# Performance work log

Measured on AMD Instinct MI355X. Metric: run time of the kernel, lower is better.

The kernel has to match this reference:

```python
import jax, jax.numpy as jnp
import numpy as np

ATOM_DIM = 64
BOND_DIM = 64
B, N_ATOMS, N_BONDS = 32, 256, 512


def setup_inputs() -> dict:
    key = jax.random.key(0)
    k1, k2, k3, k4 = jax.random.split(key, 4)
    atom_state = jax.random.normal(k1, (B, N_ATOMS, ATOM_DIM), dtype=jnp.float32)
    bond_state = jax.random.normal(k2, (B, N_BONDS, BOND_DIM), dtype=jnp.float32)
    connectivity = jax.random.randint(k3, (B, N_BONDS, 2), 0, N_ATOMS, dtype=jnp.int64)
    # glorot-ish scale for the learned bond->matrix projection
    scale = (2.0 / (BOND_DIM + ATOM_DIM * ATOM_DIM)) ** 0.5
    bond_transform = jax.random.normal(k4, (BOND_DIM, ATOM_DIM * ATOM_DIM), dtype=jnp.float32) * scale
    return {
        "atom_state": atom_state,
        "bond_state": bond_state,
        "connectivity": connectivity,
        "bond_transform": bond_transform,
    }


def reference(atom_state, bond_state, connectivity, bond_transform):
    # src atom per edge: gather along atom axis with batch dim (tf.gather batch_dims=1)
    src_idx = connectivity[:, :, 0]                                  # [B, E]
    src_atoms = jnp.take_along_axis(
        atom_state, src_idx[:, :, None], axis=1)                    # [B, E, D]
    # bond embedding -> per-edge DxD matrix
    W = bond_transform.reshape(BOND_DIM, ATOM_DIM, ATOM_DIM)         # [K, D, D]
    bond_weights = jnp.einsum('bek,kij->beij', bond_state, W)        # [B, E, D, D]
    # per-edge matrix-vector message: A_e @ h_src
    messages = jnp.einsum('beij,bej->bei', bond_weights, src_atoms)  # [B, E, D]
    return messages
```

## Files before the change

### kernel.cpp

```cpp
#include <hip/hip_runtime.h>
#include <stdint.h>


#define NATOMS 256
#define DIM 64
#define BM 64

typedef _Float16 f16;
typedef _Float16 f16x2 __attribute__((ext_vector_type(2)));
typedef _Float16 f16x8 __attribute__((ext_vector_type(8)));
typedef float f32x16 __attribute__((ext_vector_type(16)));

#define AS1 __attribute__((address_space(1)))
#define AS3 __attribute__((address_space(3)))

union H8 { f16x8 v8; f16x2 v2[4]; };

static __device__ __forceinline__ void gll16(const void* g, void* l) {
    __builtin_amdgcn_global_load_lds((AS1 void*)(uintptr_t)g, (AS3 void*)l, 16, 0, 0);
}

__global__ __launch_bounds__(256) void prep_w2f(const float* __restrict__ bt,
                                                f16* __restrict__ w2f) {
    const int d  = blockIdx.x * 256 + threadIdx.x;
    const int kg = d >> 9, c = d & 511;
    const int wcq = c >> 8, s = (c >> 6) & 3, l = c & 63;
    const int i = (l & 31) + 32 * wcq;
    const int u = 2 * s + (l >> 5);
    const float* src = bt + (size_t)kg * 4096 + i * 64 + u * 8;
    const float4 p = *reinterpret_cast<const float4*>(src);
    const float4 q = *reinterpret_cast<const float4*>(src + 4);
    const f16x8 h = { (f16)p.x, (f16)p.y, (f16)p.z, (f16)p.w,
                      (f16)q.x, (f16)q.y, (f16)q.z, (f16)q.w };
    reinterpret_cast<f16x8*>(w2f)[d] = h;
}

__global__ __launch_bounds__(512) void bond_msg(
    const float* __restrict__ atom, const float* __restrict__ bond,
    const int* __restrict__ conn, const f16* __restrict__ w2f,
    float* __restrict__ out)
{
    __shared__ __align__(16) unsigned char smem[65536];

    const int tid  = threadIdx.x;
    const int lane = tid & 63;
    const int w    = tid >> 6;
    const int wc   = w & 1;
    const int kq   = w >> 1;
    const int lo   = lane & 31;
    const int hi   = lane >> 5;
    const int blk  = blockIdx.x;
    const int bond0 = blk * BM;

    const int m0 = lo, m1 = lo + 32;
    const int ia0 = conn[(bond0 + m0) * 2];
    const int ia1 = conn[(bond0 + m1) * 2];
    const float* ar0 = atom + (size_t)(blk >> 3) * (NATOMS * DIM) + (size_t)ia0 * DIM;
    const float* ar1 = atom + (size_t)(blk >> 3) * (NATOMS * DIM) + (size_t)ia1 * DIM;
    f16x2 srcv[2][4][4];
    #pragma unroll
    for (int s = 0; s < 4; ++s) {
        const int j0 = s * 16 + hi * 8;
        float4 p0 = *reinterpret_cast<const float4*>(ar0 + j0);
        float4 p1 = *reinterpret_cast<const float4*>(ar0 + j0 + 4);
        float4 q0 = *reinterpret_cast<const float4*>(ar1 + j0);
        float4 q1 = *reinterpret_cast<const float4*>(ar1 + j0 + 4);
        srcv[0][s][0] = (f16x2){ (f16)p0.x, (f16)p0.y };
        srcv[0][s][1] = (f16x2){ (f16)p0.z, (f16)p0.w };
        srcv[0][s][2] = (f16x2){ (f16)p1.x, (f16)p1.y };
        srcv[0][s][3] = (f16x2){ (f16)p1.z, (f16)p1.w };
        srcv[1][s][0] = (f16x2){ (f16)q0.x, (f16)q0.y };
        srcv[1][s][1] = (f16x2){ (f16)q0.z, (f16)q0.w };
        srcv[1][s][2] = (f16x2){ (f16)q1.x, (f16)q1.y };
        srcv[1][s][3] = (f16x2){ (f16)q1.z, (f16)q1.w };
    }

    {
        const char* gb = reinterpret_cast<const char*>(bond + (size_t)bond0 * DIM);
        #pragma unroll
        for (int c = 0; c < 2; ++c)
            gll16(gb + w * 2048 + c * 1024 + lane * 16, smem + w * 2048 + c * 1024);
    }
    __syncthreads();
    {
        const float* bl = reinterpret_cast<const float*>(smem);
        unsigned* btw = reinterpret_cast<unsigned*>(smem + 49152);
        const int k = lane;
        #pragma unroll
        for (int mm = 0; mm < 8; ++mm) {
            const int m = w * 8 + mm;
            const f16 hh = (f16)bl[m * 64 + k];
            const f16x2 d = { hh, hh };
            btw[k * 64 + (m ^ (k & 31))] = __builtin_bit_cast(unsigned, d);
        }
    }
    __syncthreads();

    const unsigned* btl = reinterpret_cast<const unsigned*>(smem + 49152);
    const char* gw = reinterpret_cast<const char*>(w2f)
                   + (size_t)kq * 16 * 8192 + wc * 4096 + lane * 16;

    f16x8 b0[4], b1[4], b2[4], b3[4];
    f32x16 acc0, acc1;
    f16x2 pA0, pA1, pB0, pB1;

    #define LOADIT(buf, itw) do {                                         \
        const char* _p = gw + (itw) * 8192;                               \
        buf[0] = *reinterpret_cast<const f16x8*>(_p);                     \
        buf[1] = *reinterpret_cast<const f16x8*>(_p + 1024);              \
        buf[2] = *reinterpret_cast<const f16x8*>(_p + 2048);              \
        buf[3] = *reinterpret_cast<const f16x8*>(_p + 3072);              \
    } while (0)

    #define BLOAD(d0, d1, iti) do {                                      \
        const int _kg = kq * 16 + ((iti) & 15);                          \
        d0 = __builtin_bit_cast(f16x2, btl[_kg * 64 + (m0 ^ (_kg & 31))]);\
        d1 = __builtin_bit_cast(f16x2, btl[_kg * 64 + (m1 ^ (_kg & 31))]);\
    } while (0)

    #define COMPIT(buf, cb0, cb1, nb0, nb1, itn) do {                     \
        BLOAD(nb0, nb1, itn);                                             \
        _Pragma("unroll")                                                 \
        for (int s = 0; s < 4; ++s) {                                     \
            H8 _a0, _a1;                                                  \
            _Pragma("unroll")                                             \
            for (int t = 0; t < 4; ++t) {                                 \
                _a0.v2[t] = cb0 * srcv[0][s][t];                          \
                _a1.v2[t] = cb1 * srcv[1][s][t];                          \
            }                                                             \
            acc0 = __builtin_amdgcn_mfma_f32_32x32x16_f16(_a0.v8, buf[s], acc0, 0, 0, 0); \
            acc1 = __builtin_amdgcn_mfma_f32_32x32x16_f16(_a1.v8, buf[s], acc1, 0, 0, 0); \
        }                                                                 \
    } while (0)

    LOADIT(b0, 0); LOADIT(b1, 1); LOADIT(b2, 2);
    BLOAD(pA0, pA1, 0);
    acc0 = (f32x16){}; acc1 = (f32x16){};

    for (int it = 0; it < 16; it += 4) {
        LOADIT(b3, (it + 3) & 15);
        COMPIT(b0, pA0, pA1, pB0, pB1, it + 1);
        LOADIT(b0, (it + 4) & 15);
        COMPIT(b1, pB0, pB1, pA0, pA1, it + 2);
        LOADIT(b1, (it + 5) & 15);
        COMPIT(b2, pA0, pA1, pB0, pB1, it + 3);
        LOADIT(b2, (it + 6) & 15);
        COMPIT(b3, pB0, pB1, pA0, pA1, it + 4);
    }

    if (kq != 0) {
        const unsigned rbase = (unsigned)(((kq - 1) * 2 + wc) * 8192);
        #pragma unroll
        for (int g = 0; g < 4; ++g) {
            float4 v0 = { acc0[4*g+0], acc0[4*g+1], acc0[4*g+2], acc0[4*g+3] };
            *reinterpret_cast<float4*>(smem + rbase + g*1024 + lane*16) = v0;
            float4 v1 = { acc1[4*g+0], acc1[4*g+1], acc1[4*g+2], acc1[4*g+3] };
            *reinterpret_cast<float4*>(smem + rbase + (g+4)*1024 + lane*16) = v1;
        }
    }
    __syncthreads();
    if (kq == 0) {
        #pragma unroll
        for (int q = 0; q < 3; ++q) {
            const unsigned rbase = (unsigned)((q * 2 + wc) * 8192);
            #pragma unroll
            for (int g = 0; g < 4; ++g) {
                float4 v0 = *reinterpret_cast<const float4*>(smem + rbase + g*1024 + lane*16);
                acc0[4*g+0] += v0.x; acc0[4*g+1] += v0.y; acc0[4*g+2] += v0.z; acc0[4*g+3] += v0.w;
                float4 v1 = *reinterpret_cast<const float4*>(smem + rbase + (g+4)*1024 + lane*16);
                acc1[4*g+0] += v1.x; acc1[4*g+1] += v1.y; acc1[4*g+2] += v1.z; acc1[4*g+3] += v1.w;
            }
        }
        const int colb = 32 * wc + lo;
        #pragma unroll
        for (int r = 0; r < 16; ++r) {
            const int rl = (r & 3) + 8 * (r >> 2) + 4 * hi;
            out[(size_t)(bond0 + rl) * 64 + colb]      = acc0[r];
            out[(size_t)(bond0 + 32 + rl) * 64 + colb] = acc1[r];
        }
    }
    #undef LOADIT
    #undef BLOAD
    #undef COMPIT
}

__global__ __launch_bounds__(256) void bond_fallback(
    const float* __restrict__ atom, const float* __restrict__ bond,
    const int* __restrict__ conn, const float* __restrict__ bt,
    float* __restrict__ out)
{
    __shared__ float Wk[4096];
    __shared__ float srcs[4][64];
    __shared__ float bnds[4][64];
    const int blk = blockIdx.x;
    const int e0 = blk * 4;
    const int b = e0 >> 9;
    const int t = threadIdx.x;
    const int il = t & 63, eg = t >> 6;
    const int e = e0 + eg;
    const int ia = conn[e * 2];
    srcs[eg][il] = atom[(size_t)b * (NATOMS * DIM) + (size_t)ia * DIM + il];
    bnds[eg][il] = bond[(size_t)e * DIM + il];
    float acc = 0.f;
    for (int k = 0; k < 64; ++k) {
        __syncthreads();
        #pragma unroll
        for (int c = 0; c < 4; ++c) {
            float4 v = reinterpret_cast<const float4*>(bt + (size_t)k * 4096)[t + c * 256];
            reinterpret_cast<float4*>(Wk)[t + c * 256] = v;
        }
        __syncthreads();
        float s = 0.f;
        #pragma unroll
        for (int j = 0; j < 64; ++j) s += Wk[il * 64 + j] * srcs[eg][j];
        acc += bnds[eg][k] * s;
    }
    out[(size_t)e * DIM + il] = acc;
}

extern "C" void kernel_launch(void* const* d_in, const int* in_sizes, int n_in,
                              void* d_out, int out_size, void* d_ws, size_t ws_size,
                              hipStream_t stream) {
    const float* atom = (const float*)d_in[0];
    const float* bond = (const float*)d_in[1];
    const int*   conn = (const int*)d_in[2];
    const float* bt   = (const float*)d_in[3];
    float* out = (float*)d_out;

    if (ws_size >= (size_t)64 * 4096 * sizeof(f16)) {
        f16* w2f = (f16*)d_ws;
        prep_w2f<<<128, 256, 0, stream>>>(bt, w2f);
        bond_msg<<<256, 512, 0, stream>>>(atom, bond, conn, w2f, out);
    } else {
        bond_fallback<<<4096, 256, 0, stream>>>(atom, bond, conn, bt, out);
    }
}
```

Before: 23.60 us.

## Load bond coefficients into registers and parallelize K-split reduction across all waves

Bond-state coefficients are now read directly from global memory into per-thread registers. This replaces the staging through LDS plus a transpose, and removes two block-wide barriers before the MFMA loop. The main loop is fully unrolled without wraparound loads, and occupancy is hinted at two blocks per CU. The K-split partial sums are written to swizzled LDS by every wave, and the final reduction and store are spread across all 512 threads instead of only the kq==0 waves. The trade-off is higher register pressure from 32 extra f16x2 values per thread.

```diff
diff --git a/kernel.cpp b/kernel.cpp
--- a/kernel.cpp
+++ b/kernel.cpp
@@ -11,14 +11,7 @@
 typedef _Float16 f16x8 __attribute__((ext_vector_type(8)));
 typedef float f32x16 __attribute__((ext_vector_type(16)));
 
-#define AS1 __attribute__((address_space(1)))
-#define AS3 __attribute__((address_space(3)))
-
 union H8 { f16x8 v8; f16x2 v2[4]; };
-
-static __device__ __forceinline__ void gll16(const void* g, void* l) {
-    __builtin_amdgcn_global_load_lds((AS1 void*)(uintptr_t)g, (AS3 void*)l, 16, 0, 0);
-}
 
 __global__ __launch_bounds__(256) void prep_w2f(const float* __restrict__ bt,
                                                 f16* __restrict__ w2f) {
@@ -35,7 +28,11 @@
     reinterpret_cast<f16x8*>(w2f)[d] = h;
 }
 
-__global__ __launch_bounds__(512) void bond_msg(
+static __device__ __forceinline__ unsigned swz16(unsigned lane) {
+    return (lane * 16u) ^ ((lane & 0x38u) << 1);
+}
+
+__global__ __launch_bounds__(512, 2) void bond_msg(
     const float* __restrict__ atom, const float* __restrict__ bond,
     const int* __restrict__ conn, const f16* __restrict__ w2f,
     float* __restrict__ out)
@@ -55,6 +52,24 @@
     const int m0 = lo, m1 = lo + 32;
     const int ia0 = conn[(bond0 + m0) * 2];
     const int ia1 = conn[(bond0 + m1) * 2];
+
+    f16x2 bp0[16], bp1[16];
+    {
+        const float* br0 = bond + (size_t)(bond0 + m0) * DIM + kq * 16;
+        const float* br1 = bond + (size_t)(bond0 + m1) * DIM + kq * 16;
+        #pragma unroll
+        for (int q = 0; q < 4; ++q) {
+            const float4 v0 = *reinterpret_cast<const float4*>(br0 + q * 4);
+            const float4 v1 = *reinterpret_cast<const float4*>(br1 + q * 4);
+            const f16 a0 = (f16)v0.x, a1 = (f16)v0.y, a2 = (f16)v0.z, a3 = (f16)v0.w;
+            const f16 c0 = (f16)v1.x, c1 = (f16)v1.y, c2 = (f16)v1.z, c3 = (f16)v1.w;
+            bp0[q*4+0] = (f16x2){a0,a0}; bp0[q*4+1] = (f16x2){a1,a1};
+            bp0[q*4+2] = (f16x2){a2,a2}; bp0[q*4+3] = (f16x2){a3,a3};
+            bp1[q*4+0] = (f16x2){c0,c0}; bp1[q*4+1] = (f16x2){c1,c1};
+            bp1[q*4+2] = (f16x2){c2,c2}; bp1[q*4+3] = (f16x2){c3,c3};
+        }
+    }
+
     const float* ar0 = atom + (size_t)(blk >> 3) * (NATOMS * DIM) + (size_t)ia0 * DIM;
     const float* ar1 = atom + (size_t)(blk >> 3) * (NATOMS * DIM) + (size_t)ia1 * DIM;
     f16x2 srcv[2][4][4];
@@ -75,58 +90,30 @@
         srcv[1][s][3] = (f16x2){ (f16)q1.z, (f16)q1.w };
     }
 
-    {
-        const char* gb = reinterpret_cast<const char*>(bond + (size_t)bond0 * DIM);
-        #pragma unroll
-        for (int c = 0; c < 2; ++c)
-            gll16(gb + w * 2048 + c * 1024 + lane * 16, smem + w * 2048 + c * 1024);
-    }
-    __syncthreads();
-    {
-        const float* bl = reinterpret_cast<const float*>(smem);
-        unsigned* btw = reinterpret_cast<unsigned*>(smem + 49152);
-        const int k = lane;
-        #pragma unroll
-        for (int mm = 0; mm < 8; ++mm) {
-            const int m = w * 8 + mm;
-            const f16 hh = (f16)bl[m * 64 + k];
-            const f16x2 d = { hh, hh };
-            btw[k * 64 + (m ^ (k & 31))] = __builtin_bit_cast(unsigned, d);
-        }
-    }
-    __syncthreads();
-
-    const unsigned* btl = reinterpret_cast<const unsigned*>(smem + 49152);
     const char* gw = reinterpret_cast<const char*>(w2f)
                    + (size_t)kq * 16 * 8192 + wc * 4096 + lane * 16;
 
     f16x8 b0[4], b1[4], b2[4], b3[4];
-    f32x16 acc0, acc1;
-    f16x2 pA0, pA1, pB0, pB1;
-
-    #define LOADIT(buf, itw) do {                                         \
+    f32x16 acc0 = {}, acc1 = {};
+
+    #define LOADIT(buf, itw) do { if ((itw) < 16) {                       \
         const char* _p = gw + (itw) * 8192;                               \
         buf[0] = *reinterpret_cast<const f16x8*>(_p);                     \
         buf[1] = *reinterpret_cast<const f16x8*>(_p + 1024);              \
         buf[2] = *reinterpret_cast<const f16x8*>(_p + 2048);              \
         buf[3] = *reinterpret_cast<const f16x8*>(_p + 3072);              \
-    } while (0)
-
-    #define BLOAD(d0, d1, iti) do {                                      \
-        const int _kg = kq * 16 + ((iti) & 15);                          \
-        d0 = __builtin_bit_cast(f16x2, btl[_kg * 64 + (m0 ^ (_kg & 31))]);\
-        d1 = __builtin_bit_cast(f16x2, btl[_kg * 64 + (m1 ^ (_kg & 31))]);\
-    } while (0)
-
-    #define COMPIT(buf, cb0, cb1, nb0, nb1, itn) do {                     \
-        BLOAD(nb0, nb1, itn);                                             \
+    } } while (0)
+
+    #define COMPIT(buf, iti) do {                                         \
+        const f16x2 _c0 = bp0[iti];                                       \
+        const f16x2 _c1 = bp1[iti];                                       \
         _Pragma("unroll")                                                 \
         for (int s = 0; s < 4; ++s) {                                     \
             H8 _a0, _a1;                                                  \
             _Pragma("unroll")                                             \
             for (int t = 0; t < 4; ++t) {                                 \
-                _a0.v2[t] = cb0 * srcv[0][s][t];                          \
-                _a1.v2[t] = cb1 * srcv[1][s][t];                          \
+                _a0.v2[t] = _c0 * srcv[0][s][t];                          \
+                _a1.v2[t] = _c1 * srcv[1][s][t];                          \
             }                                                             \
             acc0 = __builtin_amdgcn_mfma_f32_32x32x16_f16(_a0.v8, buf[s], acc0, 0, 0, 0); \
             acc1 = __builtin_amdgcn_mfma_f32_32x32x16_f16(_a1.v8, buf[s], acc1, 0, 0, 0); \
@@ -134,53 +121,53 @@
     } while (0)
 
     LOADIT(b0, 0); LOADIT(b1, 1); LOADIT(b2, 2);
-    BLOAD(pA0, pA1, 0);
-    acc0 = (f32x16){}; acc1 = (f32x16){};
-
+
+    #pragma unroll
     for (int it = 0; it < 16; it += 4) {
-        LOADIT(b3, (it + 3) & 15);
-        COMPIT(b0, pA0, pA1, pB0, pB1, it + 1);
-        LOADIT(b0, (it + 4) & 15);
-        COMPIT(b1, pB0, pB1, pA0, pA1, it + 2);
-        LOADIT(b1, (it + 5) & 15);
-        COMPIT(b2, pA0, pA1, pB0, pB1, it + 3);
-        LOADIT(b2, (it + 6) & 15);
-        COMPIT(b3, pB0, pB1, pA0, pA1, it + 4);
-    }
-
-    if (kq != 0) {
-        const unsigned rbase = (unsigned)(((kq - 1) * 2 + wc) * 8192);
+        LOADIT(b3, it + 3);
+        COMPIT(b0, it + 0);
+        LOADIT(b0, it + 4);
+        COMPIT(b1, it + 1);
+        LOADIT(b1, it + 5);
+        COMPIT(b2, it + 2);
+        LOADIT(b2, it + 6);
+        COMPIT(b3, it + 3);
+    }
+
+    {
+        const unsigned wbase = (unsigned)w * 8192u;
+        const unsigned so = swz16((unsigned)lane);
         #pragma unroll
         for (int g = 0; g < 4; ++g) {
             float4 v0 = { acc0[4*g+0], acc0[4*g+1], acc0[4*g+2], acc0[4*g+3] };
-            *reinterpret_cast<float4*>(smem + rbase + g*1024 + lane*16) = v0;
+            *reinterpret_cast<float4*>(smem + wbase + g*1024 + so) = v0;
             float4 v1 = { acc1[4*g+0], acc1[4*g+1], acc1[4*g+2], acc1[4*g+3] };
-            *reinterpret_cast<float4*>(smem + rbase + (g+4)*1024 + lane*16) = v1;
+            *reinterpret_cast<float4*>(smem + wbase + (g+4)*1024 + so) = v1;
         }
     }
     __syncthreads();
-    if (kq == 0) {
-        #pragma unroll
-        for (int q = 0; q < 3; ++q) {
-            const unsigned rbase = (unsigned)((q * 2 + wc) * 8192);
-            #pragma unroll
-            for (int g = 0; g < 4; ++g) {
-                float4 v0 = *reinterpret_cast<const float4*>(smem + rbase + g*1024 + lane*16);
-                acc0[4*g+0] += v0.x; acc0[4*g+1] += v0.y; acc0[4*g+2] += v0.z; acc0[4*g+3] += v0.w;
-                float4 v1 = *reinterpret_cast<const float4*>(smem + rbase + (g+4)*1024 + lane*16);
-                acc1[4*g+0] += v1.x; acc1[4*g+1] += v1.y; acc1[4*g+2] += v1.z; acc1[4*g+3] += v1.w;
-            }
-        }
-        const int colb = 32 * wc + lo;
-        #pragma unroll
-        for (int r = 0; r < 16; ++r) {
-            const int rl = (r & 3) + 8 * (r >> 2) + 4 * hi;
-            out[(size_t)(bond0 + rl) * 64 + colb]      = acc0[r];
-            out[(size_t)(bond0 + 32 + rl) * 64 + colb] = acc1[r];
-        }
+    {
+        const int c  = tid & 63;
+        const int rb = tid >> 6;
+        const int a  = rb >> 2, g = rb & 3;
+        const unsigned colb = (unsigned)(c & 31);
+        const unsigned wcs  = (unsigned)(c >> 5);
+        const unsigned o0 = swz16(colb);
+        const unsigned o1 = swz16(32u + colb);
+        float4 s0 = {0.f,0.f,0.f,0.f}, s1 = {0.f,0.f,0.f,0.f};
+        #pragma unroll
+        for (int q = 0; q < 4; ++q) {
+            const unsigned base = (unsigned)((q*2 + wcs) * 8192 + (a*4+g) * 1024);
+            const float4 u0 = *reinterpret_cast<const float4*>(smem + base + o0);
+            const float4 u1 = *reinterpret_cast<const float4*>(smem + base + o1);
+            s0.x += u0.x; s0.y += u0.y; s0.z += u0.z; s0.w += u0.w;
+            s1.x += u1.x; s1.y += u1.y; s1.z += u1.z; s1.w += u1.w;
+        }
+        float* orow = out + (size_t)(bond0 + 32*a + 8*g) * 64 + c;
+        orow[0*64] = s0.x; orow[1*64] = s0.y; orow[2*64] = s0.z; orow[3*64] = s0.w;
+        orow[4*64] = s1.x; orow[5*64] = s1.y; orow[6*64] = s1.z; orow[7*64] = s1.w;
     }
     #undef LOADIT
-    #undef BLOAD
     #undef COMPIT
 }
 
```

Measured after the change: 22.92 us. 1.03x faster.
